# Kernel optimization log

Hardware: AMD Instinct MI355X
Metric: run time of the kernel (lower is better)

Reference implementation:

```python
import jax, jax.numpy as jnp
import numpy as np

WS = 8      # window_size
NH = 4      # num_heads (fixed in module)

def setup_inputs() -> dict:
    key = jax.random.key(0)
    k1, k2, k3 = jax.random.split(key, 3)
    B, C, H, W = 8, 512, 128, 128
    x = jax.random.normal(k1, (B, C, H, W), dtype=jnp.float32)
    # nn.MultiheadAttention parameters (xavier-ish scale)
    w_in = jax.random.normal(k2, (3 * C, C), dtype=jnp.float32) * (1.0 / np.sqrt(C))
    b_in = jnp.zeros((3 * C,), dtype=jnp.float32)
    w_out = jax.random.normal(k3, (C, C), dtype=jnp.float32) * (1.0 / np.sqrt(C))
    b_out = jnp.zeros((C,), dtype=jnp.float32)
    return {"x": x, "w_in": w_in, "b_in": b_in, "w_out": w_out, "b_out": b_out}

def reference(x, w_in, b_in, w_out, b_out):
    B, C, H, W = x.shape
    Hw, Ww = H // WS, W // WS
    hd = C // NH
    # --- window partition: (B,C,H,W) -> (N, L, C), N = B*Hw*Ww, L = WS*WS ---
    xw = x.reshape(B, C, Hw, WS, Ww, WS)
    xw = xw.transpose(0, 2, 4, 1, 3, 5)            # (B,Hw,Ww,C,WS,WS)
    xw = xw.reshape(-1, C, WS * WS)                # (N, C, L)
    xw = xw.transpose(0, 2, 1)                     # (N, L, C)
    N, L, _ = xw.shape
    # --- fused QKV projection (torch MultiheadAttention in_proj) ---
    qkv = jnp.einsum('nlc,ec->nle', xw, w_in) + b_in   # (N, L, 3C)
    q, k, v = jnp.split(qkv, 3, axis=-1)
    q = q.reshape(N, L, NH, hd)
    k = k.reshape(N, L, NH, hd)
    v = v.reshape(N, L, NH, hd)
    scale = 1.0 / np.sqrt(hd)
    scores = jnp.einsum('nqhd,nkhd->nhqk', q, k) * scale   # (N,NH,L,L)
    attn = jax.nn.softmax(scores, axis=-1)
    ctx = jnp.einsum('nhqk,nkhd->nqhd', attn, v).reshape(N, L, C)
    out = jnp.einsum('nlc,oc->nlo', ctx, w_out) + b_out    # (N, L, C)
    # --- window merge: (N,L,C) -> (B,C,H,W) ---
    out = out.transpose(0, 2, 1)                           # (N, C, L)
    out = out.reshape(B, Hw, Ww, C, WS, WS)
    out = out.transpose(0, 3, 1, 4, 2, 5)                  # (B,C,Hw,WS,Ww,WS)
    return out.reshape(B, C, H, W)
```

## Files before the change

### kernel.cpp

```cpp
#include <hip/hip_runtime.h>


typedef __attribute__((ext_vector_type(8))) short s16x8;
typedef __attribute__((ext_vector_type(4))) float f32x4;

#define C_TOT 512
#define HWIMG 128
#define CH_STRIDE (HWIMG * HWIMG)
#define NWIN 2048
#define XW_ELEMS ((size_t)NWIN * 64 * 512)
#define XW_BYTES (XW_ELEMS * 2ull)
#define WIT_ELEMS 786432ull
#define WOT_ELEMS 262144ull
#define WBF_ELEMS 1048576ull
#define WBF_BYTES (WBF_ELEMS * 2ull)
#define CTX_BYTES_FULL (XW_ELEMS * 2ull)

__device__ __forceinline__ unsigned short f2bf(float f) {
  unsigned u = __float_as_uint(f);
  u += 0x7FFFu + ((u >> 16) & 1u);
  return (unsigned short)(u >> 16);
}

__device__ __forceinline__ void gload_lds16(const void* g, void* l) {
  __builtin_amdgcn_global_load_lds(
      (const __attribute__((address_space(1))) unsigned int*)g,
      (__attribute__((address_space(3))) unsigned int*)l, 16, 0, 0);
}

__global__ void conv_w_kernel(const float* __restrict__ w_in,
                              const float* __restrict__ w_out,
                              unsigned short* __restrict__ wbf) {
  int i = blockIdx.x * blockDim.x + threadIdx.x;
  const int NIN = 3 * C_TOT * C_TOT;
  float v = (i < NIN) ? w_in[i] : w_out[i - NIN];
  wbf[i] = f2bf(v);
}

__global__ void conv_wt_kernel(const float* __restrict__ w_in,
                               const float* __restrict__ w_out,
                               unsigned short* __restrict__ wit,
                               unsigned short* __restrict__ wot) {
  int i = blockIdx.x * blockDim.x + threadIdx.x;
  const int NIN = 3 * C_TOT * C_TOT;
  if (i < NIN) {
    const int e = i >> 9, c = i & 511;
    const int t = e >> 9, rem = e & 511;
    const int h = rem >> 7, d = rem & 127;
    const int m = t * 8 + (d >> 4), l = d & 15;
    const int c8 = c >> 3, ec = c & 7;
    wit[(((size_t)(h * 24 + m) * 64 + c8) << 7) + l * 8 + ec] = f2bf(w_in[i]);
  } else {
    const int j = i - NIN;
    const int od = j >> 9, c = j & 511;
    const int m = od >> 4, l = od & 15;
    const int c8 = c >> 3, ec = c & 7;
    wot[(((size_t)m * 64 + c8) << 7) + l * 8 + ec] = f2bf(w_out[j]);
  }
}

__global__ void __launch_bounds__(256)
pack_x_kernel(const float* __restrict__ x, unsigned short* __restrict__ xw) {
  const int blk = blockIdx.x;
  const int bb  = blk >> 8;
  const int hw  = (blk >> 4) & 15;
  const int og4 = blk & 15;
  const int t   = threadIdx.x;
  const int p0  = 4 * t;
  const int r   = p0 >> 7;
  const int col0 = p0 & 127;
  const int n   = bb * 256 + hw * 16 + (col0 >> 3);
  const int tok0 = r * 8 + (col0 & 7);
  const float* xs = x + (size_t)bb * C_TOT * CH_STRIDE
                  + (size_t)hw * 1024 + p0;
  unsigned short* pw = xw + (size_t)n * 32768;
#pragma unroll
  for (int jo = 0; jo < 4; ++jo) {
    const int o = og4 * 4 + jo;
    float4 f[8];
#pragma unroll
    for (int k = 0; k < 8; ++k)
      f[k] = *(const float4*)(xs + (size_t)(8 * o + k) * CH_STRIDE);
#pragma unroll
    for (int i = 0; i < 4; ++i) {
      s16x8 pk;
      pk[0] = (short)f2bf(f[0].x); pk[1] = (short)f2bf(f[1].x);
      pk[2] = (short)f2bf(f[2].x); pk[3] = (short)f2bf(f[3].x);
      pk[4] = (short)f2bf(f[4].x); pk[5] = (short)f2bf(f[5].x);
      pk[6] = (short)f2bf(f[6].x); pk[7] = (short)f2bf(f[7].x);
      if (i == 0) {
        pk[0]=(short)f2bf(f[0].x); pk[1]=(short)f2bf(f[1].x); pk[2]=(short)f2bf(f[2].x); pk[3]=(short)f2bf(f[3].x);
        pk[4]=(short)f2bf(f[4].x); pk[5]=(short)f2bf(f[5].x); pk[6]=(short)f2bf(f[6].x); pk[7]=(short)f2bf(f[7].x);
      } else if (i == 1) {
        pk[0]=(short)f2bf(f[0].y); pk[1]=(short)f2bf(f[1].y); pk[2]=(short)f2bf(f[2].y); pk[3]=(short)f2bf(f[3].y);
        pk[4]=(short)f2bf(f[4].y); pk[5]=(short)f2bf(f[5].y); pk[6]=(short)f2bf(f[6].y); pk[7]=(short)f2bf(f[7].y);
      } else if (i == 2) {
        pk[0]=(short)f2bf(f[0].z); pk[1]=(short)f2bf(f[1].z); pk[2]=(short)f2bf(f[2].z); pk[3]=(short)f2bf(f[3].z);
        pk[4]=(short)f2bf(f[4].z); pk[5]=(short)f2bf(f[5].z); pk[6]=(short)f2bf(f[6].z); pk[7]=(short)f2bf(f[7].z);
      } else {
        pk[0]=(short)f2bf(f[0].w); pk[1]=(short)f2bf(f[1].w); pk[2]=(short)f2bf(f[2].w); pk[3]=(short)f2bf(f[3].w);
        pk[4]=(short)f2bf(f[4].w); pk[5]=(short)f2bf(f[5].w); pk[6]=(short)f2bf(f[6].w); pk[7]=(short)f2bf(f[7].w);
      }
      *(s16x8*)(pw + ((size_t)o * 64 + tok0 + i) * 8) = pk;
    }
  }
}

#define BQO 0
#define BKO 16384
#define BVO 32768
#define BXS 49152
#define BPO 49152
#define BLDS 81920

__global__ void __launch_bounds__(512, 4)
qkv_attn_kernel(const unsigned short* __restrict__ xw,
                const float* __restrict__ bin,
                const unsigned short* __restrict__ wit,
                unsigned short* __restrict__ ctx,
                int n0) {
  __shared__ __align__(16) unsigned char sm[BLDS];

  const int tid  = threadIdx.x;
  const int wv   = tid >> 6;
  const int lane = tid & 63;
  const int l15  = lane & 15;
  const int qd   = lane >> 4;
  const int swA  = (l15 & 7) << 4;

  const int blk = blockIdx.x;
  const int g   = blk & 7;
  const int q   = blk >> 3;
  const int h   = q & 3;
  const int nrel = (q >> 2) * 8 + g;
  const unsigned short* xww = xw + (size_t)(n0 + nrel) * 32768;

  const float SCALE = 0.08838834764831845f;
  const float L2E   = 1.4426950408889634f;

  f32x4 acc[3][4];
#pragma unroll
  for (int a = 0; a < 3; ++a)
#pragma unroll
    for (int b2 = 0; b2 < 4; ++b2) acc[a][b2] = (f32x4){0.f, 0.f, 0.f, 0.f};

  const unsigned short* arow[3];
  int typ[3], d128s[3];
#pragma unroll
  for (int mi = 0; mi < 3; ++mi) {
    const int d0 = 48 * wv + 16 * mi;
    const int t = d0 >> 7;
    const int d128 = d0 & 127;
    typ[mi] = t; d128s[mi] = d128;
    const int m = t * 8 + (d128 >> 4);
    arow[mi] = wit + ((size_t)(h * 24 + m) << 13) + l15 * 8;
  }

#pragma unroll
  for (int p = 0; p < 2; ++p)
    gload_lds16(xww + p * 4096 + tid * 8, &sm[BXS + p * 8192 + (wv << 10)]);
  __syncthreads();

  for (int s = 0; s < 4; ++s) {
    if (s < 3) {
#pragma unroll
      for (int p = 0; p < 2; ++p)
        gload_lds16(xww + (size_t)(s + 1) * 8192 + p * 4096 + tid * 8,
                    &sm[BXS + ((s + 1) & 1) * 16384 + p * 8192 + (wv << 10)]);
    }
    const int cur = BXS + (s & 1) * 16384;
#pragma unroll
    for (int j = 0; j < 4; ++j) {
      const int c8g = 16 * s + 4 * j + qd;
      const int lb = cur + ((4 * j + qd) << 10);
      s16x8 bx[4];
#pragma unroll
      for (int ni = 0; ni < 4; ++ni)
        bx[ni] = *(const s16x8*)(&sm[lb + (16 * ni + l15) * 16]);
#pragma unroll
      for (int mi = 0; mi < 3; ++mi) {
        const s16x8 af = *(const s16x8*)(arow[mi] + ((size_t)c8g << 7));
#pragma unroll
        for (int ni = 0; ni < 4; ++ni)
          acc[mi][ni] = __builtin_amdgcn_mfma_f32_16x16x32_bf16(af, bx[ni], acc[mi][ni], 0, 0, 0);
      }
    }
    __syncthreads();
  }

#pragma unroll
  for (int mi = 0; mi < 3; ++mi) {
    const int t = typ[mi], d128 = d128s[mi];
    const int e0 = t * 512 + h * 128 + d128 + 4 * qd;
    const float bi0 = bin[e0], bi1 = bin[e0 + 1], bi2 = bin[e0 + 2], bi3 = bin[e0 + 3];
#pragma unroll
    for (int ni = 0; ni < 4; ++ni) {
      const int tok = 16 * ni + l15;
      const unsigned short h0 = f2bf(acc[mi][ni][0] + bi0);
      const unsigned short h1 = f2bf(acc[mi][ni][1] + bi1);
      const unsigned short h2 = f2bf(acc[mi][ni][2] + bi2);
      const unsigned short h3 = f2bf(acc[mi][ni][3] + bi3);
      if (t < 2) {
        const unsigned lo = (unsigned)h0 | ((unsigned)h1 << 16);
        const unsigned hi = (unsigned)h2 | ((unsigned)h3 << 16);
        const unsigned long long pk = (unsigned long long)lo | ((unsigned long long)hi << 32);
        const int base = (t == 0) ? BQO : BKO;
        *(unsigned long long*)(&sm[base + tok * 256 + ((2 * (d128 + 4 * qd)) ^ swA)]) = pk;
      } else {
        const int vd = d128 + 4 * qd;
        *(unsigned short*)(&sm[BVO + (vd    ) * 128 + ((2 * tok) ^ (((vd    ) & 7) << 4))]) = h0;
        *(unsigned short*)(&sm[BVO + (vd + 1) * 128 + ((2 * tok) ^ (((vd + 1) & 7) << 4))]) = h1;
        *(unsigned short*)(&sm[BVO + (vd + 2) * 128 + ((2 * tok) ^ (((vd + 2) & 7) << 4))]) = h2;
        *(unsigned short*)(&sm[BVO + (vd + 3) * 128 + ((2 * tok) ^ (((vd + 3) & 7) << 4))]) = h3;
      }
    }
  }
  __syncthreads();

  if (wv < 4) {
    f32x4 s[4];
#pragma unroll
    for (int a = 0; a < 4; ++a) s[a] = (f32x4){0.f, 0.f, 0.f, 0.f};
    const int tqa = 16 * wv + l15;
#pragma unroll
    for (int ks = 0; ks < 4; ++ks) {
      const int c0 = 32 * ks + 8 * qd;
      const s16x8 aq = *(const s16x8*)(&sm[BQO + tqa * 256 + ((2 * c0) ^ swA)]);
#pragma unroll
      for (int ni = 0; ni < 4; ++ni) {
        const int tk = 16 * ni + l15;
        const s16x8 bk = *(const s16x8*)(&sm[BKO + tk * 256 + ((2 * c0) ^ swA)]);
        s[ni] = __builtin_amdgcn_mfma_f32_16x16x32_bf16(aq, bk, s[ni], 0, 0, 0);
      }
    }
    float sv[4][4];
#pragma unroll
    for (int ni = 0; ni < 4; ++ni)
#pragma unroll
      for (int i = 0; i < 4; ++i) sv[ni][i] = s[ni][i] * SCALE;
    float m[4];
#pragma unroll
    for (int i = 0; i < 4; ++i)
      m[i] = fmaxf(fmaxf(sv[0][i], sv[1][i]), fmaxf(sv[2][i], sv[3][i]));
#pragma unroll
    for (int d = 1; d < 16; d <<= 1)
#pragma unroll
      for (int i = 0; i < 4; ++i) m[i] = fmaxf(m[i], __shfl_xor(m[i], d));
    float p[4][4], sum[4] = {0.f, 0.f, 0.f, 0.f};
#pragma unroll
    for (int ni = 0; ni < 4; ++ni)
#pragma unroll
      for (int i = 0; i < 4; ++i) {
        p[ni][i] = exp2f((sv[ni][i] - m[i]) * L2E);
        sum[i] += p[ni][i];
      }
#pragma unroll
    for (int d = 1; d < 16; d <<= 1)
#pragma unroll
      for (int i = 0; i < 4; ++i) sum[i] += __shfl_xor(sum[i], d);
    float rinv[4];
#pragma unroll
    for (int i = 0; i < 4; ++i) rinv[i] = 1.0f / sum[i];
#pragma unroll
    for (int ni = 0; ni < 4; ++ni)
#pragma unroll
      for (int i = 0; i < 4; ++i) {
        const int tqr = 16 * wv + 4 * qd + i;
        const int tk = 16 * ni + l15;
        *(unsigned short*)(&sm[BPO + tqr * 128 + ((2 * tk) ^ ((tqr & 7) << 4))]) =
            f2bf(p[ni][i] * rinv[i]);
      }
  }
  __syncthreads();

  {
    const int mq = wv >> 1;
    const int nb = (wv & 1) * 4;
    f32x4 cacc[4];
#pragma unroll
    for (int a = 0; a < 4; ++a) cacc[a] = (f32x4){0.f, 0.f, 0.f, 0.f};
    const int tqa = 16 * mq + l15;
#pragma unroll
    for (int ks = 0; ks < 2; ++ks) {
      const int c0 = 32 * ks + 8 * qd;
      const s16x8 ap = *(const s16x8*)(&sm[BPO + tqa * 128 + ((2 * c0) ^ swA)]);
#pragma unroll
      for (int j = 0; j < 4; ++j) {
        const int vda = 16 * (nb + j) + l15;
        const s16x8 bv = *(const s16x8*)(&sm[BVO + vda * 128 + ((2 * c0) ^ swA)]);
        cacc[j] = __builtin_amdgcn_mfma_f32_16x16x32_bf16(ap, bv, cacc[j], 0, 0, 0);
      }
    }
    unsigned short* ctxn = ctx + (size_t)nrel * 32768;
#pragma unroll
    for (int j = 0; j < 4; ++j) {
      const int vd = 16 * (nb + j) + l15;
      const int c  = h * 128 + vd;
      const int c8 = c >> 3, e = c & 7;
#pragma unroll
      for (int i = 0; i < 4; ++i) {
        const int tq = 16 * mq + 4 * qd + i;
        ctxn[((size_t)c8 * 64 + tq) * 8 + e] = f2bf(cacc[j][i]);
      }
    }
  }
}

#define OXS 0
#define OLDS 32768

__global__ void __launch_bounds__(512, 4)
outproj_kernel(const unsigned short* __restrict__ ctx,
               const unsigned short* __restrict__ wot,
               const float* __restrict__ bout,
               float* __restrict__ out, int n0) {
  __shared__ __align__(16) unsigned char sm[OLDS];

  const int tid  = threadIdx.x;
  const int wv   = tid >> 6;
  const int lane = tid & 63;
  const int l15  = lane & 15;
  const int qd   = lane >> 4;

  const int nrel = blockIdx.x;
  const int n  = n0 + nrel;
  const int bb = n >> 8, hw = (n >> 4) & 15, ww = n & 15;
  const size_t wbase = (size_t)bb * C_TOT * CH_STRIDE
                     + (size_t)(hw * 8) * HWIMG + (size_t)(ww * 8);
  const unsigned short* ctxn = ctx + (size_t)nrel * 32768;

  f32x4 oacc[4][4];
#pragma unroll
  for (int a = 0; a < 4; ++a)
#pragma unroll
    for (int b2 = 0; b2 < 4; ++b2) oacc[a][b2] = (f32x4){0.f, 0.f, 0.f, 0.f};

  const unsigned short* orow[4];
#pragma unroll
  for (int mo = 0; mo < 4; ++mo)
    orow[mo] = wot + ((size_t)(4 * wv + mo) << 13) + l15 * 8;

#pragma unroll
  for (int p = 0; p < 2; ++p)
    gload_lds16(ctxn + p * 4096 + tid * 8, &sm[OXS + p * 8192 + (wv << 10)]);
  __syncthreads();

  for (int s = 0; s < 4; ++s) {
    if (s < 3) {
#pragma unroll
      for (int p = 0; p < 2; ++p)
        gload_lds16(ctxn + (size_t)(s + 1) * 8192 + p * 4096 + tid * 8,
                    &sm[OXS + ((s + 1) & 1) * 16384 + p * 8192 + (wv << 10)]);
    }
    const int cur = OXS + (s & 1) * 16384;
#pragma unroll
    for (int j = 0; j < 4; ++j) {
      const int c8g = 16 * s + 4 * j + qd;
      const int lb = cur + ((4 * j + qd) << 10);
      s16x8 bc[4];
#pragma unroll
      for (int ni = 0; ni < 4; ++ni)
        bc[ni] = *(const s16x8*)(&sm[lb + (16 * ni + l15) * 16]);
#pragma unroll
      for (int mo = 0; mo < 4; ++mo) {
        const s16x8 af = *(const s16x8*)(orow[mo] + ((size_t)c8g << 7));
#pragma unroll
        for (int ni = 0; ni < 4; ++ni)
          oacc[mo][ni] = __builtin_amdgcn_mfma_f32_16x16x32_bf16(af, bc[ni], oacc[mo][ni], 0, 0, 0);
      }
    }
    __syncthreads();
  }

#pragma unroll
  for (int mo = 0; mo < 4; ++mo) {
    const int od0 = 64 * wv + 16 * mo + 4 * qd;
    float bo[4];
#pragma unroll
    for (int i = 0; i < 4; ++i) bo[i] = bout[od0 + i];
#pragma unroll
    for (int ni = 0; ni < 4; ++ni) {
      const int tok = 16 * ni + l15;
      const int r = tok >> 3, cc = tok & 7;
#pragma unroll
      for (int i = 0; i < 4; ++i) {
        out[wbase + (size_t)(od0 + i) * CH_STRIDE + (size_t)r * HWIMG + cc] =
            oacc[mo][ni][i] + bo[i];
      }
    }
  }
}

#define QO    0
#define KO    16384
#define VO    32768
#define PO    49152
#define CTXO  57344
#define LDSB  73728

__global__ void __launch_bounds__(256)
pack_x_fb(const float* __restrict__ x, unsigned short* __restrict__ xw) {
  const int n  = blockIdx.x;
  const int bb = n >> 8, hw = (n >> 4) & 15, ww = n & 15;
  const size_t wbase = (size_t)bb * C_TOT * CH_STRIDE
                     + (size_t)(hw * 8) * HWIMG + (size_t)(ww * 8);
  const int tok = threadIdx.x & 63;
  const int q4  = threadIdx.x >> 6;
  const int r = tok >> 3, cc = tok & 7;
  const float* px = x + wbase + (size_t)r * HWIMG + cc;
  unsigned short* pw = xw + (size_t)n * 32768;
#pragma unroll 4
  for (int j = 0; j < 16; ++j) {
    const int o = q4 * 16 + j;
    float v[8];
#pragma unroll
    for (int k = 0; k < 8; ++k) v[k] = px[(size_t)(8 * o + k) * CH_STRIDE];
    s16x8 pk;
#pragma unroll
    for (int k = 0; k < 8; ++k) pk[k] = (short)f2bf(v[k]);
    *(s16x8*)(pw + ((size_t)o * 64 + tok) * 8) = pk;
  }
}

__global__ void __launch_bounds__(512, 2)
local_attn_kernel(const unsigned short* __restrict__ xw,
                  const float* __restrict__ bin,
                  const float* __restrict__ bout,
                  const unsigned short* __restrict__ wi,
                  const unsigned short* __restrict__ wo,
                  float* __restrict__ out) {
  __shared__ __align__(16) unsigned char sm[LDSB];
  const int tid  = threadIdx.x;
  const int wv   = tid >> 6;
  const int lane = tid & 63;
  const int l15  = lane & 15;
  const int qd   = lane >> 4;
  const int swA  = (l15 & 7) << 4;
  const int n  = blockIdx.x;
  const int bb = n >> 8;
  const int hw = (n >> 4) & 15;
  const int ww = n & 15;
  const size_t wbase = (size_t)bb * C_TOT * CH_STRIDE
                     + (size_t)(hw * 8) * HWIMG + (size_t)(ww * 8);
  const unsigned short* xww = xw + (size_t)n * 32768;
  f32x4 oacc[4][4];
#pragma unroll
  for (int a = 0; a < 4; ++a)
#pragma unroll
    for (int b2 = 0; b2 < 4; ++b2) oacc[a][b2] = (f32x4){0.f, 0.f, 0.f, 0.f};
  const float SCALE = 0.08838834764831845f;
  const float L2E   = 1.4426950408889634f;
  for (int h = 0; h < 4; ++h) {
    f32x4 acc[3][4];
#pragma unroll
    for (int a = 0; a < 3; ++a)
#pragma unroll
      for (int b2 = 0; b2 < 4; ++b2) acc[a][b2] = (f32x4){0.f, 0.f, 0.f, 0.f};
    const unsigned short* arow[3];
    int typ[3], d128s[3];
#pragma unroll
    for (int mi = 0; mi < 3; ++mi) {
      const int d0 = 48 * wv + 16 * mi;
      const int t = d0 >> 7;
      const int d128 = d0 & 127;
      typ[mi] = t; d128s[mi] = d128;
      arow[mi] = wi + (size_t)(t * 512 + h * 128 + d128 + l15) * 512;
    }
#pragma unroll 4
    for (int ks = 0; ks < 16; ++ks) {
      const int c0 = 32 * ks + 8 * qd;
      const int c8 = c0 >> 3;
      s16x8 bx[4];
#pragma unroll
      for (int ni = 0; ni < 4; ++ni)
        bx[ni] = *(const s16x8*)(xww + ((size_t)c8 * 64 + 16 * ni + l15) * 8);
#pragma unroll
      for (int mi = 0; mi < 3; ++mi) {
        const s16x8 af = *(const s16x8*)(arow[mi] + c0);
#pragma unroll
        for (int ni = 0; ni < 4; ++ni)
          acc[mi][ni] = __builtin_amdgcn_mfma_f32_16x16x32_bf16(af, bx[ni], acc[mi][ni], 0, 0, 0);
      }
    }
#pragma unroll
    for (int mi = 0; mi < 3; ++mi) {
      const int t = typ[mi], d128 = d128s[mi];
      const int e0 = t * 512 + h * 128 + d128 + 4 * qd;
      const float bi0 = bin[e0], bi1 = bin[e0 + 1], bi2 = bin[e0 + 2], bi3 = bin[e0 + 3];
#pragma unroll
      for (int ni = 0; ni < 4; ++ni) {
        const int tok = 16 * ni + l15;
        const unsigned short h0 = f2bf(acc[mi][ni][0] + bi0);
        const unsigned short h1 = f2bf(acc[mi][ni][1] + bi1);
        const unsigned short h2 = f2bf(acc[mi][ni][2] + bi2);
        const unsigned short h3 = f2bf(acc[mi][ni][3] + bi3);
        if (t < 2) {
          const unsigned lo = (unsigned)h0 | ((unsigned)h1 << 16);
          const unsigned hi = (unsigned)h2 | ((unsigned)h3 << 16);
          const unsigned long long pk = (unsigned long long)lo | ((unsigned long long)hi << 32);
          const int base = (t == 0) ? QO : KO;
          *(unsigned long long*)(&sm[base + tok * 256 + ((2 * (d128 + 4 * qd)) ^ swA)]) = pk;
        } else {
          const int vd = d128 + 4 * qd;
          *(unsigned short*)(&sm[VO + (vd    ) * 128 + ((2 * tok) ^ (((vd    ) & 7) << 4))]) = h0;
          *(unsigned short*)(&sm[VO + (vd + 1) * 128 + ((2 * tok) ^ (((vd + 1) & 7) << 4))]) = h1;
          *(unsigned short*)(&sm[VO + (vd + 2) * 128 + ((2 * tok) ^ (((vd + 2) & 7) << 4))]) = h2;
          *(unsigned short*)(&sm[VO + (vd + 3) * 128 + ((2 * tok) ^ (((vd + 3) & 7) << 4))]) = h3;
        }
      }
    }
    __syncthreads();
    if (wv < 4) {
      f32x4 s[4];
#pragma unroll
      for (int a = 0; a < 4; ++a) s[a] = (f32x4){0.f, 0.f, 0.f, 0.f};
      const int tqa = 16 * wv + l15;
#pragma unroll
      for (int ks = 0; ks < 4; ++ks) {
        const int c0 = 32 * ks + 8 * qd;
        const s16x8 aq = *(const s16x8*)(&sm[QO + tqa * 256 + ((2 * c0) ^ swA)]);
#pragma unroll
        for (int ni = 0; ni < 4; ++ni) {
          const int tk = 16 * ni + l15;
          const s16x8 bk = *(const s16x8*)(&sm[KO + tk * 256 + ((2 * c0) ^ swA)]);
          s[ni] = __builtin_amdgcn_mfma_f32_16x16x32_bf16(aq, bk, s[ni], 0, 0, 0);
        }
      }
      float sv[4][4];
#pragma unroll
      for (int ni = 0; ni < 4; ++ni)
#pragma unroll
        for (int i = 0; i < 4; ++i) sv[ni][i] = s[ni][i] * SCALE;
      float m[4];
#pragma unroll
      for (int i = 0; i < 4; ++i)
        m[i] = fmaxf(fmaxf(sv[0][i], sv[1][i]), fmaxf(sv[2][i], sv[3][i]));
#pragma unroll
      for (int d = 1; d < 16; d <<= 1)
#pragma unroll
        for (int i = 0; i < 4; ++i) m[i] = fmaxf(m[i], __shfl_xor(m[i], d));
      float p[4][4], sum[4] = {0.f, 0.f, 0.f, 0.f};
#pragma unroll
      for (int ni = 0; ni < 4; ++ni)
#pragma unroll
        for (int i = 0; i < 4; ++i) {
          p[ni][i] = exp2f((sv[ni][i] - m[i]) * L2E);
          sum[i] += p[ni][i];
        }
#pragma unroll
      for (int d = 1; d < 16; d <<= 1)
#pragma unroll
        for (int i = 0; i < 4; ++i) sum[i] += __shfl_xor(sum[i], d);
      float rinv[4];
#pragma unroll
      for (int i = 0; i < 4; ++i) rinv[i] = 1.0f / sum[i];
#pragma unroll
      for (int ni = 0; ni < 4; ++ni)
#pragma unroll
        for (int i = 0; i < 4; ++i) {
          const int tqr = 16 * wv + 4 * qd + i;
          const int tk = 16 * ni + l15;
          *(unsigned short*)(&sm[PO + tqr * 128 + ((2 * tk) ^ ((tqr & 7) << 4))]) =
              f2bf(p[ni][i] * rinv[i]);
        }
    }
    __syncthreads();
    {
      const int mq = wv >> 1;
      const int nb = (wv & 1) * 4;
      f32x4 cacc[4];
#pragma unroll
      for (int a = 0; a < 4; ++a) cacc[a] = (f32x4){0.f, 0.f, 0.f, 0.f};
      const int tqa = 16 * mq + l15;
#pragma unroll
      for (int ks = 0; ks < 2; ++ks) {
        const int c0 = 32 * ks + 8 * qd;
        const s16x8 ap = *(const s16x8*)(&sm[PO + tqa * 128 + ((2 * c0) ^ swA)]);
#pragma unroll
        for (int j = 0; j < 4; ++j) {
          const int vda = 16 * (nb + j) + l15;
          const s16x8 bv = *(const s16x8*)(&sm[VO + vda * 128 + ((2 * c0) ^ swA)]);
          cacc[j] = __builtin_amdgcn_mfma_f32_16x16x32_bf16(ap, bv, cacc[j], 0, 0, 0);
        }
      }
#pragma unroll
      for (int j = 0; j < 4; ++j)
#pragma unroll
        for (int i = 0; i < 4; ++i) {
          const int tq = 16 * mq + 4 * qd + i;
          const int vd = 16 * (nb + j) + l15;
          *(unsigned short*)(&sm[CTXO + tq * 256 + ((2 * vd) ^ ((tq & 7) << 4))]) =
              f2bf(cacc[j][i]);
        }
    }
    __syncthreads();
    {
#pragma unroll
      for (int ks = 0; ks < 4; ++ks) {
        const int c0 = 32 * ks + 8 * qd;
        s16x8 a2[4];
#pragma unroll
        for (int mo = 0; mo < 4; ++mo) {
          const int od = 64 * wv + 16 * mo + l15;
          a2[mo] = *(const s16x8*)(&wo[(size_t)od * 512 + 128 * h + c0]);
        }
        s16x8 bc[4];
#pragma unroll
        for (int ni = 0; ni < 4; ++ni) {
          const int tok = 16 * ni + l15;
          bc[ni] = *(const s16x8*)(&sm[CTXO + tok * 256 + ((2 * c0) ^ swA)]);
        }
#pragma unroll
        for (int mo = 0; mo < 4; ++mo)
#pragma unroll
          for (int ni = 0; ni < 4; ++ni)
            oacc[mo][ni] = __builtin_amdgcn_mfma_f32_16x16x32_bf16(a2[mo], bc[ni], oacc[mo][ni], 0, 0, 0);
      }
    }
  }
#pragma unroll
  for (int mo = 0; mo < 4; ++mo) {
    const int od0 = 64 * wv + 16 * mo + 4 * qd;
    float bo[4];
#pragma unroll
    for (int i = 0; i < 4; ++i) bo[i] = bout[od0 + i];
#pragma unroll
    for (int ni = 0; ni < 4; ++ni) {
      const int tok = 16 * ni + l15;
      const int r = tok >> 3, cc = tok & 7;
#pragma unroll
      for (int i = 0; i < 4; ++i) {
        out[wbase + (size_t)(od0 + i) * CH_STRIDE + (size_t)r * HWIMG + cc] =
            oacc[mo][ni][i] + bo[i];
      }
    }
  }
}

extern "C" void kernel_launch(void* const* d_in, const int* in_sizes, int n_in,
                              void* d_out, int out_size, void* d_ws, size_t ws_size,
                              hipStream_t stream) {
  const float* x     = (const float*)d_in[0];
  const float* w_in  = (const float*)d_in[1];
  const float* b_in  = (const float*)d_in[2];
  const float* w_out = (const float*)d_in[3];
  const float* b_out = (const float*)d_in[4];
  float* out = (float*)d_out;

  const size_t TIL_BYTES = (WIT_ELEMS + WOT_ELEMS) * 2ull;
  int nc = 0;
  for (int c = 1; c <= 8; c <<= 1) {
    if (ws_size >= XW_BYTES + TIL_BYTES + CTX_BYTES_FULL / (size_t)c) { nc = c; break; }
  }

  if (nc) {
    unsigned short* xwp = (unsigned short*)d_ws;
    unsigned short* wit = xwp + XW_ELEMS;
    unsigned short* wot = wit + WIT_ELEMS;
    unsigned short* ctx = wot + WOT_ELEMS;
    conv_wt_kernel<<<4096, 256, 0, stream>>>(w_in, w_out, wit, wot);
    pack_x_kernel<<<2048, 256, 0, stream>>>(x, xwp);
    const int nwc = NWIN / nc;
    for (int k = 0; k < nc; ++k) {
      qkv_attn_kernel<<<nwc * 4, 512, 0, stream>>>(xwp, b_in, wit, ctx, k * nwc);
      outproj_kernel<<<nwc, 512, 0, stream>>>(ctx, wot, b_out, out, k * nwc);
    }
  } else {
    unsigned short* xwp = (unsigned short*)d_ws;
    unsigned short* wbf = xwp + XW_ELEMS;
    conv_w_kernel<<<4096, 256, 0, stream>>>(w_in, w_out, wbf);
    pack_x_fb<<<NWIN, 256, 0, stream>>>(x, xwp);
    local_attn_kernel<<<NWIN, 512, 0, stream>>>(xwp, b_in, b_out,
                                                wbf, wbf + 786432, out);
  }
}
```

Before: 591.2 us.

## Remap QKV wave rows, use packed bf16 convert, start chunking at four

Each wave now computes the same head-dim slice for Q, K and V (d128 = 16*wv, row wv+8*mi), which removes the per-mi type/offset arrays and makes the store branch resolvable at compile time. Q/K epilogue conversion uses the hardware v_cvt_pk_bf16_f32 instruction instead of manual rounding. A redundant duplicate bf16 pack in the x packing loop is removed. The launcher now starts the chunk count at 4, so ctx workspace is smaller and more cache-resident, at the cost of more kernel launches.

```diff
diff --git a/kernel.cpp b/kernel.cpp
--- a/kernel.cpp
+++ b/kernel.cpp
@@ -13,13 +13,18 @@
 #define WIT_ELEMS 786432ull
 #define WOT_ELEMS 262144ull
 #define WBF_ELEMS 1048576ull
-#define WBF_BYTES (WBF_ELEMS * 2ull)
 #define CTX_BYTES_FULL (XW_ELEMS * 2ull)
 
 __device__ __forceinline__ unsigned short f2bf(float f) {
   unsigned u = __float_as_uint(f);
   u += 0x7FFFu + ((u >> 16) & 1u);
   return (unsigned short)(u >> 16);
+}
+
+__device__ __forceinline__ unsigned cvt_pk_bf16(float a, float b) {
+  unsigned r;
+  asm("v_cvt_pk_bf16_f32 %0, %1, %2" : "=v"(r) : "v"(a), "v"(b));
+  return r;
 }
 
 __device__ __forceinline__ void gload_lds16(const void* g, void* l) {
@@ -84,10 +89,6 @@
 #pragma unroll
     for (int i = 0; i < 4; ++i) {
       s16x8 pk;
-      pk[0] = (short)f2bf(f[0].x); pk[1] = (short)f2bf(f[1].x);
-      pk[2] = (short)f2bf(f[2].x); pk[3] = (short)f2bf(f[3].x);
-      pk[4] = (short)f2bf(f[4].x); pk[5] = (short)f2bf(f[5].x);
-      pk[6] = (short)f2bf(f[6].x); pk[7] = (short)f2bf(f[7].x);
       if (i == 0) {
         pk[0]=(short)f2bf(f[0].x); pk[1]=(short)f2bf(f[1].x); pk[2]=(short)f2bf(f[2].x); pk[3]=(short)f2bf(f[3].x);
         pk[4]=(short)f2bf(f[4].x); pk[5]=(short)f2bf(f[5].x); pk[6]=(short)f2bf(f[6].x); pk[7]=(short)f2bf(f[7].x);
@@ -144,17 +145,11 @@
 #pragma unroll
     for (int b2 = 0; b2 < 4; ++b2) acc[a][b2] = (f32x4){0.f, 0.f, 0.f, 0.f};
 
+  const int d128 = 16 * wv;
   const unsigned short* arow[3];
-  int typ[3], d128s[3];
-#pragma unroll
-  for (int mi = 0; mi < 3; ++mi) {
-    const int d0 = 48 * wv + 16 * mi;
-    const int t = d0 >> 7;
-    const int d128 = d0 & 127;
-    typ[mi] = t; d128s[mi] = d128;
-    const int m = t * 8 + (d128 >> 4);
-    arow[mi] = wit + ((size_t)(h * 24 + m) << 13) + l15 * 8;
-  }
+#pragma unroll
+  for (int mi = 0; mi < 3; ++mi)
+    arow[mi] = wit + ((size_t)(h * 24 + wv + 8 * mi) << 13) + l15 * 8;
 
 #pragma unroll
   for (int p = 0; p < 2; ++p)
@@ -190,23 +185,22 @@
 
 #pragma unroll
   for (int mi = 0; mi < 3; ++mi) {
-    const int t = typ[mi], d128 = d128s[mi];
-    const int e0 = t * 512 + h * 128 + d128 + 4 * qd;
+    const int e0 = mi * 512 + h * 128 + d128 + 4 * qd;
     const float bi0 = bin[e0], bi1 = bin[e0 + 1], bi2 = bin[e0 + 2], bi3 = bin[e0 + 3];
 #pragma unroll
     for (int ni = 0; ni < 4; ++ni) {
       const int tok = 16 * ni + l15;
-      const unsigned short h0 = f2bf(acc[mi][ni][0] + bi0);
-      const unsigned short h1 = f2bf(acc[mi][ni][1] + bi1);
-      const unsigned short h2 = f2bf(acc[mi][ni][2] + bi2);
-      const unsigned short h3 = f2bf(acc[mi][ni][3] + bi3);
-      if (t < 2) {
-        const unsigned lo = (unsigned)h0 | ((unsigned)h1 << 16);
-        const unsigned hi = (unsigned)h2 | ((unsigned)h3 << 16);
+      if (mi < 2) {
+        const unsigned lo = cvt_pk_bf16(acc[mi][ni][0] + bi0, acc[mi][ni][1] + bi1);
+        const unsigned hi = cvt_pk_bf16(acc[mi][ni][2] + bi2, acc[mi][ni][3] + bi3);
         const unsigned long long pk = (unsigned long long)lo | ((unsigned long long)hi << 32);
-        const int base = (t == 0) ? BQO : BKO;
+        const int base = (mi == 0) ? BQO : BKO;
         *(unsigned long long*)(&sm[base + tok * 256 + ((2 * (d128 + 4 * qd)) ^ swA)]) = pk;
       } else {
+        const unsigned short h0 = f2bf(acc[mi][ni][0] + bi0);
+        const unsigned short h1 = f2bf(acc[mi][ni][1] + bi1);
+        const unsigned short h2 = f2bf(acc[mi][ni][2] + bi2);
+        const unsigned short h3 = f2bf(acc[mi][ni][3] + bi3);
         const int vd = d128 + 4 * qd;
         *(unsigned short*)(&sm[BVO + (vd    ) * 128 + ((2 * tok) ^ (((vd    ) & 7) << 4))]) = h0;
         *(unsigned short*)(&sm[BVO + (vd + 1) * 128 + ((2 * tok) ^ (((vd + 1) & 7) << 4))]) = h1;
@@ -649,7 +643,7 @@
 
   const size_t TIL_BYTES = (WIT_ELEMS + WOT_ELEMS) * 2ull;
   int nc = 0;
-  for (int c = 1; c <= 8; c <<= 1) {
+  for (int c = 4; c <= 8; c <<= 1) {
     if (ws_size >= XW_BYTES + TIL_BYTES + CTX_BYTES_FULL / (size_t)c) { nc = c; break; }
   }
 
```

Result: slower. 681.5 us (+15.3%).
